# Optimization experiments

Measured on AMD Instinct MI355X. Metric: run time of the kernel, lower is better.

Reference implementation:

```python
import jax, jax.numpy as jnp
import numpy as np
from jax import lax

PATCH = 8

def setup_inputs() -> dict:
    key = jax.random.key(0)
    ks = jax.random.split(key, 5)
    x = jax.random.normal(ks[0], (4, 64, 256, 256), dtype=jnp.float32)
    w_in = jax.random.normal(ks[1], (512, 64), dtype=jnp.float32) * 0.02
    b_in = jnp.zeros((512,), dtype=jnp.float32)
    w_dw = jax.random.normal(ks[2], (512, 1, 3, 3), dtype=jnp.float32) * 0.02
    b_dw = jnp.zeros((512,), dtype=jnp.float32)
    w_out = jax.random.normal(ks[3], (64, 256), dtype=jnp.float32) * 0.02
    b_out = jnp.zeros((64,), dtype=jnp.float32)
    fft_filter = jnp.ones((64, 1, 1, PATCH, PATCH // 2 + 1), dtype=jnp.float32)
    return {"x": x, "w_in": w_in, "b_in": b_in, "w_dw": w_dw, "b_dw": b_dw,
            "w_out": w_out, "b_out": b_out, "fft_filter": fft_filter}

def reference(x, w_in, b_in, w_dw, b_dw, w_out, b_out, fft_filter):
    # project_in: 1x1 conv == channel GEMM. x: [B, C, H, W] -> [B, 2h, H, W]
    h = jnp.einsum('oc,bchw->bohw', w_in, x) + b_in[None, :, None, None]
    # depthwise 3x3 conv, padding=1
    h = lax.conv_general_dilated(
        h, w_dw, window_strides=(1, 1), padding='SAME',
        dimension_numbers=('NCHW', 'OIHW', 'NCHW'),
        feature_group_count=w_dw.shape[0]) + b_dw[None, :, None, None]
    x1, x2 = jnp.split(h, 2, axis=1)
    h = jax.nn.gelu(x1, approximate=False) * x2  # exact GELU like F.gelu
    # project_out: 1x1 conv
    y = jnp.einsum('oc,bchw->bohw', w_out, h) + b_out[None, :, None, None]
    # patch-wise spectral filtering
    B, C, H, W = y.shape
    p = PATCH
    yp = y.reshape(B, C, H // p, p, W // p, p).transpose(0, 1, 2, 4, 3, 5)  # b c h w p1 p2
    yf = jnp.fft.rfft2(yp)              # b c h w p1 (p2//2+1)
    yf = yf * fft_filter                # filter broadcasts over (c,1,1,p1,p2r)
    yp = jnp.fft.irfft2(yf, s=(p, p))
    y = yp.transpose(0, 1, 2, 4, 3, 5).reshape(B, C, H, W)
    return y
```

## Files before the change

kernel.cpp:

```cpp
#include <hip/hip_runtime.h>
#include <math.h>

typedef __attribute__((ext_vector_type(8))) short short8;
typedef __attribute__((ext_vector_type(4))) float f32x4;
typedef __attribute__((ext_vector_type(2))) float f32x2;
typedef _Float16 f16x8 __attribute__((ext_vector_type(8)));

#define TILE 16
#define IH 256
#define IW 256

#define WSA_OFF 16384
#define WSC_OFF 81920

#define H_STRIDE 1456
#define G_OFF 23296
#define G_BUF 16384
#define SMEM_BYTES 56064

__device__ __forceinline__ unsigned short f2bf(float f) {
  unsigned int u = __builtin_bit_cast(unsigned int, f);
  u = (u + 0x7FFFu + ((u >> 16) & 1u)) >> 16;
  return (unsigned short)u;
}

__global__ void edffn_prep(const float* __restrict__ fftf,
                           const float* __restrict__ w_in,
                           const float* __restrict__ w_out,
                           float* __restrict__ ws) {
  int blk = blockIdx.x, t = threadIdx.x;
  if (blk < 64) {
    int a = t >> 3, bb = t & 7;
    const float c0 = 0.70710678118654752f;
    const float ctab[8] = {1.f, c0, 0.f, -c0, -1.f, -c0, 0.f, c0};
    const float* F = fftf + blk * 40;
    float acc = 0.f;
    for (int k1 = 0; k1 < 8; ++k1)
      for (int k2 = 0; k2 < 8; ++k2) {
        float f = (k2 <= 4) ? F[k1 * 5 + k2] : F[((8 - k1) & 7) * 5 + (8 - k2)];
        acc += f * ctab[(k1 * a + k2 * bb) & 7];
      }
    ws[blk * 64 + t] = acc * (1.f / 64.f);
  } else if (blk < 128) {
    int b2 = blk - 64;
    int q = b2 >> 2, s = (b2 >> 1) & 1, ks = b2 & 1;
    int row = (s ? 256 : 0) + q * 16 + (t & 15);
    unsigned short* dst =
        (unsigned short*)((unsigned char*)ws + WSA_OFF) + (((q * 2 + s) * 2 + ks) * 64 + t) * 8;
    for (int j = 0; j < 8; ++j) {
      int k = ks * 32 + (t >> 4) * 8 + j;
      dst[j] = f2bf(w_in[row * 64 + k]);
    }
  } else {
    int b3 = blk - 128;
    int p = b3 >> 2, mt = b3 & 3;
    int row = mt * 16 + (t & 15);
    unsigned short* dst =
        (unsigned short*)((unsigned char*)ws + WSC_OFF) + ((p * 4 + mt) * 64 + t) * 8;
    for (int j = 0; j < 8; ++j) {
      int k = p * 32 + (t >> 4) * 8 + j;
      _Float16 hv = (_Float16)w_out[row * 256 + k];
      dst[j] = __builtin_bit_cast(unsigned short, hv);
    }
  }
}

__global__ __launch_bounds__(256, 2) void edffn_main(
    const float* __restrict__ x, const float* __restrict__ b_in,
    const float* __restrict__ w_dw, const float* __restrict__ b_dw,
    const float* __restrict__ b_out, const float* __restrict__ ws,
    float* __restrict__ out) {
  __shared__ __align__(16) unsigned char smem[SMEM_BYTES];
  __shared__ int s_flag;
  const int t = threadIdx.x;
  const int lane = t & 63, wave = t >> 6;
  const int l15 = lane & 15, lg = lane >> 4;
  const int gx0 = blockIdx.x * TILE, gy0 = blockIdx.y * TILE;
  const int b = blockIdx.z;
  const unsigned short* wsA = (const unsigned short*)((const unsigned char*)ws + WSA_OFF);
  const unsigned short* wsC = (const unsigned short*)((const unsigned char*)ws + WSC_OFF);

  short8 xf[6][2];
  int haddr[6];
  unsigned vmask = 0, imask = 0;
  const float* xb = x + (size_t)b * 64 * 65536;
#pragma unroll
  for (int i = 0; i < 6; ++i) {
    int nt = wave + 4 * i;
    int n = nt * 16 + l15;
    int hy = n / 18;
    int hx = n - hy * 18;
    int gy = gy0 + hy - 1, gx = gx0 + hx - 1;
    int vnt = (nt < 21) & (n < 324);
    int inb = vnt & (gy >= 0) & (gy < IH) & (gx >= 0) & (gx < IW);
    haddr[i] = hy * 80 + hx * 4;
    vmask |= (unsigned)vnt << i;
    imask |= (unsigned)inb << i;
    int gyc = min(max(gy, 0), IH - 1), gxc = min(max(gx, 0), IW - 1);
    const float* xp = xb + (size_t)gyc * IW + gxc;
#pragma unroll
    for (int ks = 0; ks < 2; ++ks) {
#pragma unroll
      for (int j = 0; j < 8; ++j) {
        int k = ks * 32 + lg * 8 + j;
        unsigned short bf = f2bf(xp[(size_t)k * 65536]);
        xf[i][ks][j] = (short)(inb ? bf : (unsigned short)0);
      }
    }
  }

  f32x4 accY[16];
#pragma unroll
  for (int i = 0; i < 16; ++i) accY[i] = (f32x4){0.f, 0.f, 0.f, 0.f};

  const int cp_dw = t & 15;
  const int oy_dw = t >> 4;

  auto loadWD = [&](int qq, unsigned (&wd)[9], unsigned& bd) {
    const int cg1 = qq * 16 + cp_dw, cg2 = 256 + qq * 16 + cp_dw;
#pragma unroll
    for (int u = 0; u < 9; ++u) {
      float w1 = w_dw[cg1 * 9 + u], w2 = w_dw[cg2 * 9 + u];
      asm("v_cvt_pkrtz_f16_f32 %0, %1, %2" : "=v"(wd[u]) : "v"(w1), "v"(w2));
    }
    float b1 = b_dw[cg1], b2 = b_dw[cg2];
    asm("v_cvt_pkrtz_f16_f32 %0, %1, %2" : "=v"(bd) : "v"(b1), "v"(b2));
  };

#define PKC(nm, val)                                                        \
  unsigned nm;                                                              \
  {                                                                         \
    float fv = (val);                                                       \
    asm("v_cvt_pkrtz_f16_f32 %0, %1, %1" : "=v"(nm) : "v"(fv));             \
  }
  PKC(kSQ, 0.70710678f)
  PKC(kC216, 1.f / 216.f)
  PKC(kCm42, -1.f / 42.f)
  PKC(kC10, 0.1f)
  PKC(kCm3, -1.f / 3.f)
  PKC(kOne, 1.0f)
  PKC(kHalf, 0.5f)
  PKC(kErf, 1.12837917f)
#undef PKC

  unsigned wdC[9], wdN[9], bdC, bdN;
  f16x8 cfC;
  loadWD(0, wdC, bdC);
  cfC = *(const f16x8*)(wsC + ((0 * 4 + wave) * 64 + lane) * 8);

  for (int q = 0; q < 16; ++q) {
    {
      short8 af[2][2];
#pragma unroll
      for (int s = 0; s < 2; ++s)
#pragma unroll
        for (int ks = 0; ks < 2; ++ks)
          af[s][ks] = *(const short8*)(wsA + (((q * 2 + s) * 2 + ks) * 64 + lane) * 8);
      float bin[2][4];
#pragma unroll
      for (int s = 0; s < 2; ++s)
#pragma unroll
        for (int r = 0; r < 4; ++r) bin[s][r] = b_in[(s ? 256 : 0) + q * 16 + lg * 4 + r];
#pragma unroll
      for (int i = 0; i < 6; ++i) {
        if (wave + 4 * i < 21) {
          f32x4 acc0 = {0.f, 0.f, 0.f, 0.f}, acc1 = {0.f, 0.f, 0.f, 0.f};
          acc0 = __builtin_amdgcn_mfma_f32_16x16x32_bf16(af[0][0], xf[i][0], acc0, 0, 0, 0);
          acc0 = __builtin_amdgcn_mfma_f32_16x16x32_bf16(af[0][1], xf[i][1], acc0, 0, 0, 0);
          acc1 = __builtin_amdgcn_mfma_f32_16x16x32_bf16(af[1][0], xf[i][0], acc1, 0, 0, 0);
          acc1 = __builtin_amdgcn_mfma_f32_16x16x32_bf16(af[1][1], xf[i][1], acc1, 0, 0, 0);
          if ((vmask >> i) & 1u) {
            unsigned keep = (imask >> i) & 1u;
#pragma unroll
            for (int r = 0; r < 4; ++r) {
              float v0 = acc0[r] + bin[0][r];
              float v1 = acc1[r] + bin[1][r];
              unsigned pk;
              asm("v_cvt_pkrtz_f16_f32 %0, %1, %2" : "=v"(pk) : "v"(v0), "v"(v1));
              pk = keep ? pk : 0u;
              *(unsigned*)(smem + (lg * 4 + r) * H_STRIDE + haddr[i]) = pk;
            }
          }
        }
      }
    }
    if (q < 15) loadWD(q + 1, wdN, bdN);
    __syncthreads();

    if (q >= 2 && !(q & 1)) {
      const int pc = (q >> 1) - 1;
      const unsigned short* G =
          (const unsigned short*)(smem + G_OFF + (pc & 1) * G_BUF);
#pragma unroll
      for (int nt = 0; nt < 16; ++nt) {
        int g = lg ^ (nt & 3);
        int n = nt * 16 + l15;
        f16x8 bf = *(const f16x8*)(G + n * 32 + g * 8);
        accY[nt] = __builtin_amdgcn_mfma_f32_16x16x32_f16(cfC, bf, accY[nt], 0, 0, 0);
      }
      cfC = *(const f16x8*)(wsC + (((pc + 1) * 4 + wave) * 64 + lane) * 8);
    }

    {
      const int cp = cp_dw, oy = oy_dw;
      unsigned a[16];
#pragma unroll
      for (int j = 0; j < 16; ++j) a[j] = bdC;
#pragma unroll
      for (int dy = 0; dy < 3; ++dy) {
        const uint4* rp = (const uint4*)(smem + cp * H_STRIDE + (oy + dy) * 80);
        uint4 r0 = rp[0], r1 = rp[1], r2 = rp[2], r3 = rp[3];
        uint2 r4 = ((const uint2*)rp)[8];
        unsigned e[18] = {r0.x, r0.y, r0.z, r0.w, r1.x, r1.y, r1.z, r1.w,
                          r2.x, r2.y, r2.z, r2.w, r3.x, r3.y, r3.z, r3.w,
                          r4.x, r4.y};
#pragma unroll
        for (int ox = 0; ox < 16; ++ox) {
#pragma unroll
          for (int dx = 0; dx < 3; ++dx)
            asm("v_pk_fma_f16 %0, %1, %2, %0"
                : "+v"(a[ox])
                : "v"(wdC[dy * 3 + dx]), "v"(e[ox + dx]));
        }
      }
      const int c2 = (q & 1) * 16 + cp;
      const int gi = (c2 >> 3) ^ (oy & 3);
      unsigned short* Gp = (unsigned short*)(smem + G_OFF + ((q >> 1) & 1) * G_BUF) +
                           oy * 16 * 32 + gi * 8 + (c2 & 7);
      unsigned umax = 0;
      unsigned gw[8];
#pragma unroll
      for (int j = 0; j < 8; ++j) {
        unsigned a0 = a[2 * j], a1 = a[2 * j + 1];
        unsigned u = __builtin_amdgcn_perm(a1, a0, 0x05040100u);
        unsigned v = __builtin_amdgcn_perm(a1, a0, 0x07060302u);
        unsigned uabs = u & 0x7FFF7FFFu;
        asm("v_pk_max_f16 %0, %1, %2" : "=v"(umax) : "v"(umax), "v"(uabs));
        unsigned z, z2, p, erfv, tt, g;
        asm("v_pk_mul_f16 %0, %1, %2" : "=v"(z) : "v"(u), "v"(kSQ));
        asm("v_pk_mul_f16 %0, %1, %2" : "=v"(z2) : "v"(z), "v"(z));
        asm("v_pk_fma_f16 %0, %1, %2, %3" : "=v"(p) : "v"(z2), "v"(kC216), "v"(kCm42));
        asm("v_pk_fma_f16 %0, %1, %2, %3" : "=v"(p) : "v"(z2), "v"(p), "v"(kC10));
        asm("v_pk_fma_f16 %0, %1, %2, %3" : "=v"(p) : "v"(z2), "v"(p), "v"(kCm3));
        asm("v_pk_fma_f16 %0, %1, %2, %3" : "=v"(p) : "v"(z2), "v"(p), "v"(kOne));
        asm("v_pk_mul_f16 %0, %1, %2" : "=v"(erfv) : "v"(z), "v"(p));
        asm("v_pk_mul_f16 %0, %1, %2" : "=v"(erfv) : "v"(erfv), "v"(kErf));
        asm("v_pk_fma_f16 %0, %1, %2, %2" : "=v"(tt) : "v"(erfv), "v"(kHalf));
        asm("v_pk_mul_f16 %0, %1, %2" : "=v"(g) : "v"(u), "v"(tt));
        asm("v_pk_mul_f16 %0, %1, %2" : "=v"(g) : "v"(g), "v"(v));
        gw[j] = g;
      }
      {
        float m0, m1;
        unsigned uh = umax >> 16;
        asm("v_cvt_f32_f16 %0, %1" : "=v"(m0) : "v"(umax));
        asm("v_cvt_f32_f16 %0, %1" : "=v"(m1) : "v"(uh));
        if (__builtin_expect(fmaxf(m0, m1) > 0.565685f, 0)) {
#pragma unroll
          for (int j = 0; j < 8; ++j) {
            float g01[2];
#pragma unroll
            for (int kx = 0; kx < 2; ++kx) {
              unsigned aw = a[2 * j + kx], ah = aw >> 16;
              float hu, hv2;
              asm("v_cvt_f32_f16 %0, %1" : "=v"(hu) : "v"(aw));
              asm("v_cvt_f32_f16 %0, %1" : "=v"(hv2) : "v"(ah));
              g01[kx] = 0.5f * hu * (1.f + erff(hu * 0.70710678f)) * hv2;
            }
            unsigned pk;
            asm("v_cvt_pkrtz_f16_f32 %0, %1, %2" : "=v"(pk) : "v"(g01[0]), "v"(g01[1]));
            gw[j] = pk;
          }
        }
      }
#pragma unroll
      for (int j = 0; j < 8; ++j) {
        Gp[(2 * j) * 32] = (unsigned short)gw[j];
        Gp[(2 * j + 1) * 32] = (unsigned short)(gw[j] >> 16);
      }
    }
    __syncthreads();

    if (q < 15) {
#pragma unroll
      for (int u = 0; u < 9; ++u) wdC[u] = wdN[u];
      bdC = bdN;
    }
  }

  {
    const unsigned short* G = (const unsigned short*)(smem + G_OFF + G_BUF);
#pragma unroll
    for (int nt = 0; nt < 16; ++nt) {
      int g = lg ^ (nt & 3);
      int n = nt * 16 + l15;
      f16x8 bf = *(const f16x8*)(G + n * 32 + g * 8);
      accY[nt] = __builtin_amdgcn_mfma_f32_16x16x32_f16(cfC, bf, accY[nt], 0, 0, 0);
    }
  }

  {
    f32x4 bo;
#pragma unroll
    for (int r = 0; r < 4; ++r) bo[r] = b_out[wave * 16 + lg * 4 + r];
#pragma unroll
    for (int nt = 0; nt < 16; ++nt)
#pragma unroll
      for (int r = 0; r < 4; ++r) accY[nt][r] += bo[r];
  }

  if (t == 0) s_flag = 1;
  __syncthreads();
  {
    int ok = 1;
    const float* kc = ws;
#pragma unroll
    for (int j = 0; j < 16; ++j) {
      int idx = t * 16 + j;
      float e = ((idx & 63) == 0) ? 1.f : 0.f;
      ok &= (fabsf(kc[idx] - e) <= 1e-5f) ? 1 : 0;
    }
    if (!ok) s_flag = 0;
  }
  __syncthreads();

  const int o = wave * 16 + lg * 4;
  if (s_flag) {
#pragma unroll
    for (int nt = 0; nt < 16; ++nt) {
      float* op = out + (((size_t)(b * 64 + o)) * IH + gy0 + nt) * IW + gx0 + l15;
#pragma unroll
      for (int r = 0; r < 4; ++r) op[(size_t)r * IH * IW] = accY[nt][r];
    }
    return;
  }

  float* YS = (float*)smem;
  for (int half = 0; half < 2; ++half) {
    __syncthreads();
    if ((wave >> 1) == half) {
      int c32 = (wave & 1) * 16 + lg * 4;
#pragma unroll
      for (int nt = 0; nt < 16; ++nt)
#pragma unroll
        for (int r = 0; r < 4; ++r) YS[(c32 + r) * 260 + nt * 16 + l15] = accY[nt][r];
    }
    __syncthreads();
    if (t < 128) {
      int o32 = t >> 2, oo = half * 32 + o32, qd = t & 3;
      const float* kp = ws + oo * 64;
      int py0 = (qd >> 1) * 8, px0 = (qd & 1) * 8;
      const float* row = YS + o32 * 260;
      for (int i = 0; i < 8; ++i)
        for (int j = 0; j < 8; ++j) {
          float acc = 0.f;
          for (int a_ = 0; a_ < 8; ++a_)
            for (int b_ = 0; b_ < 8; ++b_)
              acc += kp[a_ * 8 + b_] *
                     row[(py0 + ((i - a_) & 7)) * 16 + px0 + ((j - b_) & 7)];
          out[(((size_t)(b * 64 + oo)) * IH + gy0 + py0 + i) * IW + gx0 + px0 + j] = acc;
        }
    }
  }
}

extern "C" void kernel_launch(void* const* d_in, const int* in_sizes, int n_in,
                              void* d_out, int out_size, void* d_ws, size_t ws_size,
                              hipStream_t stream) {
  const float* x = (const float*)d_in[0];
  const float* w_in = (const float*)d_in[1];
  const float* b_in = (const float*)d_in[2];
  const float* w_dw = (const float*)d_in[3];
  const float* b_dw = (const float*)d_in[4];
  const float* w_out = (const float*)d_in[5];
  const float* b_out = (const float*)d_in[6];
  const float* fftf = (const float*)d_in[7];
  float* out = (float*)d_out;
  float* ws = (float*)d_ws;

  edffn_prep<<<160, 64, 0, stream>>>(fftf, w_in, w_out, ws);
  dim3 grid(IW / TILE, IH / TILE, 4);
  edffn_main<<<grid, 256, 0, stream>>>(x, b_in, w_dw, b_dw, b_out, ws, out);
}
```

Before: 150.2 us.

## Double-buffer project-in tile and spread project-out MFMAs across iterations

Project-in results go into two LDS buffers, so stage A for the next channel chunk runs after the depthwise/GELU stage of the current one. This drops one __syncthreads per iteration. The project-out GEMM is split into halves of 8 tiles issued on every iteration instead of 16 tiles on every other one, which evens out MFMA work. LDS use grows from about 56 KB to 79 KB per block, which may lower occupancy.

```diff
diff --git a/kernel.cpp b/kernel.cpp
--- a/kernel.cpp
+++ b/kernel.cpp
@@ -14,9 +14,10 @@
 #define WSC_OFF 81920
 
 #define H_STRIDE 1456
-#define G_OFF 23296
+#define H_BUF 23296
+#define G_OFF 46592
 #define G_BUF 16384
-#define SMEM_BYTES 56064
+#define SMEM_BYTES 79360
 
 __device__ __forceinline__ unsigned short f2bf(float f) {
   unsigned int u = __builtin_bit_cast(unsigned int, f);
@@ -127,11 +128,48 @@
     asm("v_cvt_pkrtz_f16_f32 %0, %1, %2" : "=v"(bd) : "v"(b1), "v"(b2));
   };
 
-#define PKC(nm, val)                                                        \
-  unsigned nm;                                                              \
-  {                                                                         \
-    float fv = (val);                                                       \
-    asm("v_cvt_pkrtz_f16_f32 %0, %1, %1" : "=v"(nm) : "v"(fv));             \
+  auto stageA = [&](int qq) {
+    short8 af[2][2];
+#pragma unroll
+    for (int s = 0; s < 2; ++s)
+#pragma unroll
+      for (int ks = 0; ks < 2; ++ks)
+        af[s][ks] = *(const short8*)(wsA + (((qq * 2 + s) * 2 + ks) * 64 + lane) * 8);
+    float bin[2][4];
+#pragma unroll
+    for (int s = 0; s < 2; ++s)
+#pragma unroll
+      for (int r = 0; r < 4; ++r) bin[s][r] = b_in[(s ? 256 : 0) + qq * 16 + lg * 4 + r];
+    unsigned char* Hb = smem + (qq & 1) * H_BUF;
+#pragma unroll
+    for (int i = 0; i < 6; ++i) {
+      if (wave + 4 * i < 21) {
+        f32x4 acc0 = {0.f, 0.f, 0.f, 0.f}, acc1 = {0.f, 0.f, 0.f, 0.f};
+        acc0 = __builtin_amdgcn_mfma_f32_16x16x32_bf16(af[0][0], xf[i][0], acc0, 0, 0, 0);
+        acc0 = __builtin_amdgcn_mfma_f32_16x16x32_bf16(af[0][1], xf[i][1], acc0, 0, 0, 0);
+        acc1 = __builtin_amdgcn_mfma_f32_16x16x32_bf16(af[1][0], xf[i][0], acc1, 0, 0, 0);
+        acc1 = __builtin_amdgcn_mfma_f32_16x16x32_bf16(af[1][1], xf[i][1], acc1, 0, 0, 0);
+        if ((vmask >> i) & 1u) {
+          unsigned keep = (imask >> i) & 1u;
+#pragma unroll
+          for (int r = 0; r < 4; ++r) {
+            float v0 = acc0[r] + bin[0][r];
+            float v1 = acc1[r] + bin[1][r];
+            unsigned pk;
+            asm("v_cvt_pkrtz_f16_f32 %0, %1, %2" : "=v"(pk) : "v"(v0), "v"(v1));
+            pk = keep ? pk : 0u;
+            *(unsigned*)(Hb + (lg * 4 + r) * H_STRIDE + haddr[i]) = pk;
+          }
+        }
+      }
+    }
+  };
+
+#define PKC(nm, val)                                            \
+  unsigned nm;                                                  \
+  {                                                             \
+    float fv = (val);                                           \
+    asm("v_cvt_pkrtz_f16_f32 %0, %1, %1" : "=v"(nm) : "v"(fv)); \
   }
   PKC(kSQ, 0.70710678f)
   PKC(kC216, 1.f / 216.f)
@@ -148,67 +186,39 @@
   loadWD(0, wdC, bdC);
   cfC = *(const f16x8*)(wsC + ((0 * 4 + wave) * 64 + lane) * 8);
 
+  stageA(0);
+  __syncthreads();
+
   for (int q = 0; q < 16; ++q) {
-    {
-      short8 af[2][2];
-#pragma unroll
-      for (int s = 0; s < 2; ++s)
-#pragma unroll
-        for (int ks = 0; ks < 2; ++ks)
-          af[s][ks] = *(const short8*)(wsA + (((q * 2 + s) * 2 + ks) * 64 + lane) * 8);
-      float bin[2][4];
-#pragma unroll
-      for (int s = 0; s < 2; ++s)
-#pragma unroll
-        for (int r = 0; r < 4; ++r) bin[s][r] = b_in[(s ? 256 : 0) + q * 16 + lg * 4 + r];
-#pragma unroll
-      for (int i = 0; i < 6; ++i) {
-        if (wave + 4 * i < 21) {
-          f32x4 acc0 = {0.f, 0.f, 0.f, 0.f}, acc1 = {0.f, 0.f, 0.f, 0.f};
-          acc0 = __builtin_amdgcn_mfma_f32_16x16x32_bf16(af[0][0], xf[i][0], acc0, 0, 0, 0);
-          acc0 = __builtin_amdgcn_mfma_f32_16x16x32_bf16(af[0][1], xf[i][1], acc0, 0, 0, 0);
-          acc1 = __builtin_amdgcn_mfma_f32_16x16x32_bf16(af[1][0], xf[i][0], acc1, 0, 0, 0);
-          acc1 = __builtin_amdgcn_mfma_f32_16x16x32_bf16(af[1][1], xf[i][1], acc1, 0, 0, 0);
-          if ((vmask >> i) & 1u) {
-            unsigned keep = (imask >> i) & 1u;
-#pragma unroll
-            for (int r = 0; r < 4; ++r) {
-              float v0 = acc0[r] + bin[0][r];
-              float v1 = acc1[r] + bin[1][r];
-              unsigned pk;
-              asm("v_cvt_pkrtz_f16_f32 %0, %1, %2" : "=v"(pk) : "v"(v0), "v"(v1));
-              pk = keep ? pk : 0u;
-              *(unsigned*)(smem + (lg * 4 + r) * H_STRIDE + haddr[i]) = pk;
-            }
-          }
-        }
-      }
-    }
-    if (q < 15) loadWD(q + 1, wdN, bdN);
-    __syncthreads();
-
-    if (q >= 2 && !(q & 1)) {
-      const int pc = (q >> 1) - 1;
+    if (q >= 2) {
+      const int h = q - 2;
+      const int p = h >> 1;
+      const int nt0 = (h & 1) * 8;
       const unsigned short* G =
-          (const unsigned short*)(smem + G_OFF + (pc & 1) * G_BUF);
-#pragma unroll
-      for (int nt = 0; nt < 16; ++nt) {
+          (const unsigned short*)(smem + G_OFF + (p & 1) * G_BUF);
+#pragma unroll
+      for (int k = 0; k < 8; ++k) {
+        int nt = nt0 + k;
         int g = lg ^ (nt & 3);
         int n = nt * 16 + l15;
         f16x8 bf = *(const f16x8*)(G + n * 32 + g * 8);
         accY[nt] = __builtin_amdgcn_mfma_f32_16x16x32_f16(cfC, bf, accY[nt], 0, 0, 0);
       }
-      cfC = *(const f16x8*)(wsC + (((pc + 1) * 4 + wave) * 64 + lane) * 8);
-    }
+      if (h & 1)
+        cfC = *(const f16x8*)(wsC + (((p + 1) * 4 + wave) * 64 + lane) * 8);
+    }
+
+    if (q < 15) loadWD(q + 1, wdN, bdN);
 
     {
       const int cp = cp_dw, oy = oy_dw;
+      const unsigned char* Hb = smem + (q & 1) * H_BUF;
       unsigned a[16];
 #pragma unroll
       for (int j = 0; j < 16; ++j) a[j] = bdC;
 #pragma unroll
       for (int dy = 0; dy < 3; ++dy) {
-        const uint4* rp = (const uint4*)(smem + cp * H_STRIDE + (oy + dy) * 80);
+        const uint4* rp = (const uint4*)(Hb + cp * H_STRIDE + (oy + dy) * 80);
         uint4 r0 = rp[0], r1 = rp[1], r2 = rp[2], r3 = rp[3];
         uint2 r4 = ((const uint2*)rp)[8];
         unsigned e[18] = {r0.x, r0.y, r0.z, r0.w, r1.x, r1.y, r1.z, r1.w,
@@ -279,13 +289,15 @@
         Gp[(2 * j + 1) * 32] = (unsigned short)(gw[j] >> 16);
       }
     }
-    __syncthreads();
+
+    if (q < 15) stageA(q + 1);
 
     if (q < 15) {
 #pragma unroll
       for (int u = 0; u < 9; ++u) wdC[u] = wdN[u];
       bdC = bdN;
     }
+    __syncthreads();
   }
 
   {
```

After: 260.6 us. +73.6%, slower.
